# Kernel tuning notes

Hardware: AMD Instinct MI355X
Metric: run time of the kernel (lower is better)

Reference implementation:

```python
import jax, jax.numpy as jnp
import numpy as np

N_SH, N_U, N_I = 1195, 805, 390   # hard-coded in KDHR
D = 64                            # embedding_dim / latent_dim
B = 65536                         # prescription batch
E_SH = 100000
BN_EPS = 1e-5


def setup_inputs() -> dict:
    key = jax.random.key(0)
    ks = jax.random.split(key, 20)
    s = 0.02
    return {
        "edge_index_SH": jax.random.randint(ks[0], (2, E_SH), 0, N_SH),
        "edge_index_SS": jax.random.randint(ks[1], (2, 50000), 0, N_U),
        "edge_index_HH": jax.random.randint(ks[2], (2, 50000), 0, N_I),
        "prescription": jax.random.uniform(ks[3], (B, N_I), dtype=jnp.float32),
        "sh_emb": jax.random.normal(ks[4], (N_SH, D), dtype=jnp.float32) * s,
        # GCNConv_SH layer 1 and 2 (Linear weights, torch layout [out,in])
        "W1": jax.random.normal(ks[5], (D, D), dtype=jnp.float32) * s,
        "b1": jnp.zeros((D,), jnp.float32),
        "W2": jax.random.normal(ks[6], (D, D), dtype=jnp.float32) * s,
        "b2": jnp.zeros((D,), jnp.float32),
        # proj = Linear(64,64) -> ELU -> Linear(64,64)
        "Wp1": jax.random.normal(ks[7], (D, D), dtype=jnp.float32) * s,
        "bp1": jnp.zeros((D,), jnp.float32),
        "Wp2": jax.random.normal(ks[8], (D, D), dtype=jnp.float32) * s,
        "bp2": jnp.zeros((D,), jnp.float32),
        # self.mlp = Linear(64,64); self.SI_bn = BatchNorm1d(64)
        "Wm": jax.random.normal(ks[9], (D, D), dtype=jnp.float32) * s,
        "bm": jnp.zeros((D,), jnp.float32),
        "bn_gamma": jnp.ones((D,), jnp.float32),
        "bn_beta": jnp.zeros((D,), jnp.float32),
    }


def _gcn_layer(x, W, b, src, dst):
    # GCNConv_SH: message = lin(x_j), aggr='mean' at dst, then tanh
    m = x[src] @ W.T + b                                   # [E, D]
    s = jax.ops.segment_sum(m, dst, num_segments=N_SH)     # [N_SH, D]
    cnt = jax.ops.segment_sum(jnp.ones(dst.shape, x.dtype), dst, num_segments=N_SH)
    return jnp.tanh(s / jnp.maximum(cnt, 1.0)[:, None])


def _l2n(z):
    return z / jnp.linalg.norm(z, axis=1, keepdims=True)


def reference(edge_index_SH, edge_index_SS, edge_index_HH, prescription,
              sh_emb, W1, b1, W2, b2, Wp1, bp1, Wp2, bp2, Wm, bm,
              bn_gamma, bn_beta):
    src, dst = edge_index_SH[0], edge_index_SH[1]
    h1 = _gcn_layer(sh_emb, W1, b1, src, dst)
    h2 = _gcn_layer(h1, W2, b2, src, dst)                  # x_SH6
    c_emb_u, c_emb_i = h2[:N_U], h2[N_U:]                  # [805,64], [390,64]

    def proj(z):
        return jax.nn.elu(z @ Wp1.T + bp1) @ Wp2.T + bp2

    # Same2Loss projected+normalized embeddings (c_u: herbs 390, c_i: users 805)
    es = _l2n(proj(c_emb_i))                               # [390, 64]
    eh = _l2n(proj(c_emb_u))                               # [805, 64]

    e_synd = prescription @ es                             # [B, 64]
    pre_sum = jnp.sum(prescription, axis=1, keepdims=True)
    e = e_synd / pre_sum
    e = e @ Wm.T + bm                                      # mlp
    mu = jnp.mean(e, axis=0)                               # BatchNorm1d (train)
    var = jnp.var(e, axis=0)
    e = (e - mu) * jax.lax.rsqrt(var + BN_EPS) * bn_gamma + bn_beta
    e = jax.nn.relu(e)
    return e @ eh.T                                        # [B, 805]
```

## Files before the change

### kernel.cpp

```cpp
#include <hip/hip_runtime.h>
#include <math.h>

#define NSH 1195
#define NU  805
#define NI  390
#define DD  64
#define BROWS 65536
#define ESH 100000
#define KPAD 416
#define NUPAD 832

typedef _Float16 f16;
typedef _Float16 f16x8 __attribute__((ext_vector_type(8)));
typedef float f32x4 __attribute__((ext_vector_type(4)));

#define OFF_AGG   0u
#define OFF_CNT   76480u
#define OFF_H1    77760u
#define OFF_H2    154240u
#define OFF_EH    230720u
#define OFF_ES    282240u
#define OFF_ESWT  307200u
#define OFF_STATS 332160u
#define OFF_BN    332288u
#define OFF_EPRE  332416u

__global__ __launch_bounds__(256) void agg_kernel(const int* __restrict__ edges,
                                                  const float* __restrict__ x,
                                                  float* __restrict__ agg,
                                                  float* __restrict__ cnt,
                                                  int do_cnt) {
    int gid = blockIdx.x * 256 + threadIdx.x;
    int e = gid >> 6;
    int d = gid & 63;
    if (e < ESH) {
        int s = edges[e];
        int t = edges[ESH + e];
        atomicAdd(&agg[t * DD + d], x[s * DD + d]);
        if (do_cnt && d == 0) atomicAdd(&cnt[t], 1.0f);
    }
}

__global__ __launch_bounds__(256) void gcn_transform(const float* __restrict__ agg,
                                                     const float* __restrict__ cnt,
                                                     const float* __restrict__ W,
                                                     const float* __restrict__ b,
                                                     float* __restrict__ out) {
    __shared__ float s_wt[DD * DD];
    __shared__ float s_z[4 * DD];
    int tid = threadIdx.x;
    for (int i = tid; i < DD * DD; i += 256) {
        int j = i >> 6, k = i & 63;
        s_wt[k * DD + j] = W[i];
    }
    int w = tid >> 6, j = tid & 63;
    int node = blockIdx.x * 4 + w;
    bool active = node < NSH;
    s_z[w * DD + j] = active ? agg[node * DD + j] : 0.f;
    __syncthreads();
    float c = active ? cnt[node] : 0.f;
    float acc = c * b[j];
    #pragma unroll 8
    for (int k = 0; k < DD; k++)
        acc = fmaf(s_z[w * DD + k], s_wt[k * DD + j], acc);
    float h = tanhf(acc / fmaxf(c, 1.0f));
    if (active) out[node * DD + j] = h;
}

__global__ __launch_bounds__(256) void proj_kernel(const float* __restrict__ h2,
                                                   const float* __restrict__ Wp1,
                                                   const float* __restrict__ bp1,
                                                   const float* __restrict__ Wp2,
                                                   const float* __restrict__ bp2,
                                                   f16* __restrict__ eh16,
                                                   float* __restrict__ es) {
    __shared__ float s_w1[DD * DD], s_w2[DD * DD];
    __shared__ float s_z[4 * DD], s_t[4 * DD];
    int tid = threadIdx.x;
    for (int i = tid; i < DD * DD; i += 256) {
        int j = i >> 6, k = i & 63;
        s_w1[k * DD + j] = Wp1[i];
        s_w2[k * DD + j] = Wp2[i];
    }
    int w = tid >> 6, j = tid & 63;
    int node = blockIdx.x * 4 + w;
    bool active = node < NSH;
    s_z[w * DD + j] = active ? h2[node * DD + j] : 0.f;
    __syncthreads();
    float acc = bp1[j];
    #pragma unroll 8
    for (int k = 0; k < DD; k++)
        acc = fmaf(s_z[w * DD + k], s_w1[k * DD + j], acc);
    float t = acc > 0.f ? acc : expm1f(acc);
    s_t[w * DD + j] = t;
    __syncthreads();
    float o = bp2[j];
    #pragma unroll 8
    for (int k = 0; k < DD; k++)
        o = fmaf(s_t[w * DD + k], s_w2[k * DD + j], o);
    float sq = o * o;
    #pragma unroll
    for (int off = 1; off < 64; off <<= 1) sq += __shfl_xor(sq, off);
    float r = o / sqrtf(sq);
    if (active) {
        if (node < NU) eh16[node * DD + j] = (f16)r;
        else           es[(node - NU) * DD + j] = r;
    }
}

__global__ __launch_bounds__(256) void projm_kernel(const float* __restrict__ es,
                                                    const float* __restrict__ Wm,
                                                    f16* __restrict__ esWT) {
    __shared__ float s_wt[DD * DD];
    __shared__ float s_z[4 * DD];
    int tid = threadIdx.x;
    for (int i = tid; i < DD * DD; i += 256) {
        int j = i >> 6, k = i & 63;
        s_wt[k * DD + j] = Wm[i];
    }
    int w = tid >> 6, j = tid & 63;
    int r = blockIdx.x * 4 + w;
    bool active = r < NI;
    s_z[w * DD + j] = active ? es[r * DD + j] : 0.f;
    __syncthreads();
    float o = 0.f;
    #pragma unroll 8
    for (int k = 0; k < DD; k++)
        o = fmaf(s_z[w * DD + k], s_wt[k * DD + j], o);
    if (active) esWT[j * KPAD + r] = (f16)o;
}

__global__ __launch_bounds__(256) void synd_mfma(const float* __restrict__ P,
                                                 const f16* __restrict__ esWT,
                                                 const float* __restrict__ bm,
                                                 float* __restrict__ e_pre,
                                                 float* __restrict__ stats) {
    __shared__ float s_stats[128];
    int tid = threadIdx.x;
    if (tid < 128) s_stats[tid] = 0.f;
    __syncthreads();
    int lane = tid & 63, wv = tid >> 6;
    int l15 = lane & 15, lk = lane >> 4;
    int rowbase = blockIdx.x * 128 + wv * 32;

    f32x4 acc[2][4];
    #pragma unroll
    for (int mi = 0; mi < 2; mi++)
        #pragma unroll
        for (int ni = 0; ni < 4; ni++)
            acc[mi][ni] = (f32x4){0.f, 0.f, 0.f, 0.f};
    float rs[2] = {0.f, 0.f};

    const float* pr[2];
    pr[0] = P + (size_t)(rowbase + l15) * NI;
    pr[1] = P + (size_t)(rowbase + 16 + l15) * NI;
    const f16* bp[4];
    #pragma unroll
    for (int ni = 0; ni < 4; ni++)
        bp[ni] = esWT + (size_t)(ni * 16 + l15) * KPAD;

    for (int step = 0; step < 12; step++) {
        int kb = step * 32 + lk * 8;
        f16x8 afr[2];
        #pragma unroll
        for (int mi = 0; mi < 2; mi++) {
            const float* p = pr[mi] + kb;
            float2 q0 = *(const float2*)(p);
            float2 q1 = *(const float2*)(p + 2);
            float2 q2 = *(const float2*)(p + 4);
            float2 q3 = *(const float2*)(p + 6);
            rs[mi] += ((q0.x + q0.y) + (q1.x + q1.y)) + ((q2.x + q2.y) + (q3.x + q3.y));
            f16x8 a;
            a[0] = (f16)q0.x; a[1] = (f16)q0.y; a[2] = (f16)q1.x; a[3] = (f16)q1.y;
            a[4] = (f16)q2.x; a[5] = (f16)q2.y; a[6] = (f16)q3.x; a[7] = (f16)q3.y;
            afr[mi] = a;
        }
        f16x8 bfr[4];
        #pragma unroll
        for (int ni = 0; ni < 4; ni++)
            bfr[ni] = *(const f16x8*)(bp[ni] + kb);
        #pragma unroll
        for (int mi = 0; mi < 2; mi++)
            #pragma unroll
            for (int ni = 0; ni < 4; ni++)
                acc[mi][ni] = __builtin_amdgcn_mfma_f32_16x16x32_f16(
                    afr[mi], bfr[ni], acc[mi][ni], 0, 0, 0);
    }
    {
        f16x8 afr[2];
        #pragma unroll
        for (int mi = 0; mi < 2; mi++) {
            f16x8 a = (f16x8)(f16)0.f;
            if (lk == 0) {
                const float* p = pr[mi] + 384;
                float2 q0 = *(const float2*)(p);
                float2 q1 = *(const float2*)(p + 2);
                float2 q2 = *(const float2*)(p + 4);
                rs[mi] += ((q0.x + q0.y) + (q1.x + q1.y)) + (q2.x + q2.y);
                a[0] = (f16)q0.x; a[1] = (f16)q0.y; a[2] = (f16)q1.x;
                a[3] = (f16)q1.y; a[4] = (f16)q2.x; a[5] = (f16)q2.y;
            }
            afr[mi] = a;
        }
        f16x8 bfr[4];
        #pragma unroll
        for (int ni = 0; ni < 4; ni++)
            bfr[ni] = *(const f16x8*)(bp[ni] + 384 + lk * 8);
        #pragma unroll
        for (int mi = 0; mi < 2; mi++)
            #pragma unroll
            for (int ni = 0; ni < 4; ni++)
                acc[mi][ni] = __builtin_amdgcn_mfma_f32_16x16x32_f16(
                    afr[mi], bfr[ni], acc[mi][ni], 0, 0, 0);
    }

    #pragma unroll
    for (int mi = 0; mi < 2; mi++) {
        rs[mi] += __shfl_xor(rs[mi], 16);
        rs[mi] += __shfl_xor(rs[mi], 32);
    }
    float rsr[2][4];
    #pragma unroll
    for (int mi = 0; mi < 2; mi++)
        #pragma unroll
        for (int j = 0; j < 4; j++)
            rsr[mi][j] = __shfl(rs[mi], lk * 4 + j);

    float bmv[4];
    #pragma unroll
    for (int ni = 0; ni < 4; ni++) bmv[ni] = bm[ni * 16 + l15];

    #pragma unroll
    for (int ni = 0; ni < 4; ni++) {
        float s = 0.f, q = 0.f;
        #pragma unroll
        for (int mi = 0; mi < 2; mi++) {
            #pragma unroll
            for (int j = 0; j < 4; j++) {
                float v = acc[mi][ni][j] / rsr[mi][j] + bmv[ni];
                int row = rowbase + mi * 16 + lk * 4 + j;
                e_pre[(size_t)row * DD + ni * 16 + l15] = v;
                s += v;
                q = fmaf(v, v, q);
            }
        }
        s += __shfl_xor(s, 16); s += __shfl_xor(s, 32);
        q += __shfl_xor(q, 16); q += __shfl_xor(q, 32);
        if (lk == 0) {
            atomicAdd(&s_stats[ni * 16 + l15], s);
            atomicAdd(&s_stats[64 + ni * 16 + l15], q);
        }
    }
    __syncthreads();
    if (tid < 128) atomicAdd(&stats[tid], s_stats[tid]);
}

#define CG0 448
__global__ __launch_bounds__(256) void out_fused(const float* __restrict__ e_pre,
                                                 const f16* __restrict__ eh16,
                                                 const float* __restrict__ stats,
                                                 const float* __restrict__ gamma,
                                                 const float* __restrict__ beta,
                                                 float* __restrict__ out) {
    __shared__ __align__(16) f16 s_eh[CG0 * DD];
    __shared__ float s_bn[128];
    int tid = threadIdx.x;
    int cg = blockIdx.x;
    int nrows = cg == 0 ? CG0 : (NUPAD - CG0);
    int cbase = cg * CG0;

    if (tid < 64) {
        float mu  = stats[tid] * (1.0f / 65536.0f);
        float ex2 = stats[64 + tid] * (1.0f / 65536.0f);
        float var = ex2 - mu * mu;
        float rstd = 1.0f / sqrtf(var + 1e-5f);
        float sc = rstd * gamma[tid];
        s_bn[tid] = sc;
        s_bn[64 + tid] = beta[tid] - mu * sc;
    }

    const uint4* src = (const uint4*)(eh16 + (size_t)cbase * DD);
    int nchunks = nrows * 8;
    for (int c = tid; c < nchunks; c += 256) {
        int row = c >> 3, slot = c & 7;
        uint4 v = src[c];
        *(uint4*)&s_eh[row * DD + ((slot ^ (row & 7)) << 3)] = v;
    }
    __syncthreads();

    int lane = tid & 63, w = tid >> 6;
    int l15 = lane & 15, lk = lane >> 4;
    int r0 = blockIdx.y * 64 + w * 16;

    f16x8 afr[2];
    {
        const float* pr = e_pre + (size_t)(r0 + l15) * DD;
        #pragma unroll
        for (int ks = 0; ks < 2; ks++) {
            int kb = ks * 32 + lk * 8;
            f32x4 v0 = *(const f32x4*)&pr[kb];
            f32x4 v1 = *(const f32x4*)&pr[kb + 4];
            f16x8 a;
            #pragma unroll
            for (int i = 0; i < 4; i++) {
                a[i]     = (f16)fmaxf(fmaf(v0[i], s_bn[kb + i],     s_bn[64 + kb + i]),     0.f);
                a[4 + i] = (f16)fmaxf(fmaf(v1[i], s_bn[kb + 4 + i], s_bn[64 + kb + 4 + i]), 0.f);
            }
            afr[ks] = a;
        }
    }

    int nt = cg == 0 ? 7 : 6;
    for (int cb = 0; cb < nt; cb += 4) {
        f32x4 acc[4][4];
        #pragma unroll
        for (int tt = 0; tt < 4; tt++)
            #pragma unroll
            for (int c16 = 0; c16 < 4; c16++)
                acc[tt][c16] = (f32x4){0.f, 0.f, 0.f, 0.f};

        #pragma unroll
        for (int tt = 0; tt < 4; tt++) {
            if (cb + tt < nt) {
                #pragma unroll
                for (int c16 = 0; c16 < 4; c16++) {
                    int lc = (cb + tt) * 64 + c16 * 16 + l15;
                    #pragma unroll
                    for (int ks = 0; ks < 2; ks++) {
                        int slot = (ks * 4 + lk) ^ (lc & 7);
                        f16x8 b = *(const f16x8*)&s_eh[lc * DD + (slot << 3)];
                        acc[tt][c16] = __builtin_amdgcn_mfma_f32_16x16x32_f16(
                            afr[ks], b, acc[tt][c16], 0, 0, 0);
                    }
                }
            }
        }
        #pragma unroll
        for (int tt = 0; tt < 4; tt++) {
            if (cb + tt < nt) {
                #pragma unroll
                for (int c16 = 0; c16 < 4; c16++) {
                    int col = cbase + (cb + tt) * 64 + c16 * 16 + l15;
                    if (col < NU) {
                        #pragma unroll
                        for (int j = 0; j < 4; j++) {
                            int row = r0 + lk * 4 + j;
                            out[(size_t)row * NU + col] = acc[tt][c16][j];
                        }
                    }
                }
            }
        }
    }
}

extern "C" void kernel_launch(void* const* d_in, const int* in_sizes, int n_in,
                              void* d_out, int out_size, void* d_ws, size_t ws_size,
                              hipStream_t stream) {
    const int*   eSH   = (const int*)d_in[0];
    const float* presc = (const float*)d_in[3];
    const float* shemb = (const float*)d_in[4];
    const float* W1  = (const float*)d_in[5];
    const float* b1  = (const float*)d_in[6];
    const float* W2  = (const float*)d_in[7];
    const float* b2  = (const float*)d_in[8];
    const float* Wp1 = (const float*)d_in[9];
    const float* bp1 = (const float*)d_in[10];
    const float* Wp2 = (const float*)d_in[11];
    const float* bp2 = (const float*)d_in[12];
    const float* Wm  = (const float*)d_in[13];
    const float* bm  = (const float*)d_in[14];
    const float* gam = (const float*)d_in[15];
    const float* bet = (const float*)d_in[16];

    float* ws    = (float*)d_ws;
    float* agg   = ws + OFF_AGG;
    float* cnt   = ws + OFF_CNT;
    float* h1    = ws + OFF_H1;
    float* h2    = ws + OFF_H2;
    f16*   eh16  = (f16*)(ws + OFF_EH);
    float* es    = ws + OFF_ES;
    f16*   esWT  = (f16*)(ws + OFF_ESWT);
    float* stats = ws + OFF_STATS;
    float* e_pre = ws + OFF_EPRE;
    float* out   = (float*)d_out;

    hipMemsetAsync(agg, 0, (76480 + 1280) * sizeof(float), stream);
    hipMemsetAsync(stats, 0, 128 * sizeof(float), stream);
    hipMemsetAsync(eh16, 0, (size_t)NUPAD * DD * sizeof(f16), stream);
    hipMemsetAsync(esWT, 0, (size_t)DD * KPAD * sizeof(f16), stream);

    agg_kernel<<<25000, 256, 0, stream>>>(eSH, shemb, agg, cnt, 1);
    gcn_transform<<<299, 256, 0, stream>>>(agg, cnt, W1, b1, h1);
    hipMemsetAsync(agg, 0, 76480 * sizeof(float), stream);
    agg_kernel<<<25000, 256, 0, stream>>>(eSH, h1, agg, cnt, 0);
    gcn_transform<<<299, 256, 0, stream>>>(agg, cnt, W2, b2, h2);
    proj_kernel<<<299, 256, 0, stream>>>(h2, Wp1, bp1, Wp2, bp2, eh16, es);
    projm_kernel<<<98, 256, 0, stream>>>(es, Wm, esWT);
    synd_mfma<<<512, 256, 0, stream>>>(presc, esWT, bm, e_pre, stats);
    out_fused<<<dim3(2, 1024), 256, 0, stream>>>(e_pre, eh16, stats, gam, bet, out);
}
```

Measured before the change: 231.7 us.

## Replace atomic edge scatter with CSR gather and fuse GCN layer 2 with projections

Builds a CSR (histogram, scan, scatter) of the SH edges once, so each node gathers its neighbours' features instead of doing 6.4M float atomics per layer. The second GCN layer, the projection MLP, the normalisation and the Wm projection are fused into one per-node kernel, and the memsets are merged into one. The cost is three small serial setup kernels, including a single-block scan, plus one block per node with possibly uneven degrees. Summation order inside each node now follows the order edges land in the CSR, not the atomic order.

```diff
diff --git a/kernel.cpp b/kernel.cpp
--- a/kernel.cpp
+++ b/kernel.cpp
@@ -14,120 +14,163 @@
 typedef _Float16 f16x8 __attribute__((ext_vector_type(8)));
 typedef float f32x4 __attribute__((ext_vector_type(4)));
 
-#define OFF_AGG   0u
-#define OFF_CNT   76480u
-#define OFF_H1    77760u
-#define OFF_H2    154240u
-#define OFF_EH    230720u
-#define OFF_ES    282240u
-#define OFF_ESWT  307200u
-#define OFF_STATS 332160u
-#define OFF_BN    332288u
-#define OFF_EPRE  332416u
-
-__global__ __launch_bounds__(256) void agg_kernel(const int* __restrict__ edges,
-                                                  const float* __restrict__ x,
-                                                  float* __restrict__ agg,
-                                                  float* __restrict__ cnt,
-                                                  int do_cnt) {
-    int gid = blockIdx.x * 256 + threadIdx.x;
-    int e = gid >> 6;
-    int d = gid & 63;
+#define OFF_STATS  0u
+#define OFF_ESWT   128u
+#define OFF_EH     13440u
+#define OFF_HIST   40064u
+#define ZERO_FLOATS 41344u
+#define OFF_ROWPTR 41344u
+#define OFF_CURSOR 42624u
+#define OFF_COLIDX 43904u
+#define OFF_H1     144000u
+#define OFF_EPRE   220480u
+
+__global__ __launch_bounds__(256) void hist_kernel(const int* __restrict__ edges,
+                                                   int* __restrict__ hist) {
+    int e = blockIdx.x * 256 + threadIdx.x;
+    if (e < ESH) atomicAdd(&hist[edges[ESH + e]], 1);
+}
+
+__global__ __launch_bounds__(1024) void scan_kernel(const int* __restrict__ hist,
+                                                    int* __restrict__ row_ptr,
+                                                    int* __restrict__ cursor) {
+    __shared__ int s[2048];
+    int t = threadIdx.x;
+    s[t] = (t < NSH) ? hist[t] : 0;
+    s[t + 1024] = (t + 1024 < NSH) ? hist[t + 1024] : 0;
+    __syncthreads();
+    for (int off = 1; off < 2048; off <<= 1) {
+        int a = s[t], b = s[t + 1024];
+        int aa = (t >= off) ? s[t - off] : 0;
+        int bb = s[t + 1024 - off];
+        __syncthreads();
+        s[t] = a + aa;
+        s[t + 1024] = b + bb;
+        __syncthreads();
+    }
+    if (t == 0) row_ptr[0] = 0;
+    for (int i = t; i < NSH; i += 1024) {
+        row_ptr[i + 1] = s[i];
+        cursor[i] = (i == 0) ? 0 : s[i - 1];
+    }
+}
+
+__global__ __launch_bounds__(256) void scatter_kernel(const int* __restrict__ edges,
+                                                      int* __restrict__ cursor,
+                                                      int* __restrict__ col_idx) {
+    int e = blockIdx.x * 256 + threadIdx.x;
     if (e < ESH) {
-        int s = edges[e];
         int t = edges[ESH + e];
-        atomicAdd(&agg[t * DD + d], x[s * DD + d]);
-        if (do_cnt && d == 0) atomicAdd(&cnt[t], 1.0f);
-    }
-}
-
-__global__ __launch_bounds__(256) void gcn_transform(const float* __restrict__ agg,
-                                                     const float* __restrict__ cnt,
-                                                     const float* __restrict__ W,
-                                                     const float* __restrict__ b,
-                                                     float* __restrict__ out) {
+        int pos = atomicAdd(&cursor[t], 1);
+        col_idx[pos] = edges[e];
+    }
+}
+
+__global__ __launch_bounds__(256) void gcn_gather1(const int* __restrict__ row_ptr,
+                                                   const int* __restrict__ col_idx,
+                                                   const float* __restrict__ x,
+                                                   const float* __restrict__ W,
+                                                   const float* __restrict__ b,
+                                                   float* __restrict__ out) {
     __shared__ float s_wt[DD * DD];
-    __shared__ float s_z[4 * DD];
+    __shared__ float s_p[4 * DD];
     int tid = threadIdx.x;
+    int w = tid >> 6, lane = tid & 63;
     for (int i = tid; i < DD * DD; i += 256) {
         int j = i >> 6, k = i & 63;
         s_wt[k * DD + j] = W[i];
     }
-    int w = tid >> 6, j = tid & 63;
-    int node = blockIdx.x * 4 + w;
-    bool active = node < NSH;
-    s_z[w * DD + j] = active ? agg[node * DD + j] : 0.f;
-    __syncthreads();
-    float c = active ? cnt[node] : 0.f;
-    float acc = c * b[j];
+    int node = blockIdx.x;
+    int beg = row_ptr[node], end = row_ptr[node + 1];
+    float acc = 0.f;
+    for (int e = beg + w; e < end; e += 4)
+        acc += x[col_idx[e] * DD + lane];
+    s_p[w * DD + lane] = acc;
+    __syncthreads();
+    float z = s_p[lane] + s_p[DD + lane] + s_p[2 * DD + lane] + s_p[3 * DD + lane];
+    __syncthreads();
+    if (w == 0) s_p[lane] = z;
+    __syncthreads();
+    float cntf = (float)(end - beg);
+    float o = cntf * b[lane];
     #pragma unroll 8
     for (int k = 0; k < DD; k++)
-        acc = fmaf(s_z[w * DD + k], s_wt[k * DD + j], acc);
-    float h = tanhf(acc / fmaxf(c, 1.0f));
-    if (active) out[node * DD + j] = h;
-}
-
-__global__ __launch_bounds__(256) void proj_kernel(const float* __restrict__ h2,
-                                                   const float* __restrict__ Wp1,
-                                                   const float* __restrict__ bp1,
-                                                   const float* __restrict__ Wp2,
-                                                   const float* __restrict__ bp2,
-                                                   f16* __restrict__ eh16,
-                                                   float* __restrict__ es) {
-    __shared__ float s_w1[DD * DD], s_w2[DD * DD];
-    __shared__ float s_z[4 * DD], s_t[4 * DD];
+        o = fmaf(s_p[k], s_wt[k * DD + lane], o);
+    float h = tanhf(o / fmaxf(cntf, 1.f));
+    if (w == 0) out[node * DD + lane] = h;
+}
+
+__global__ __launch_bounds__(256) void gcn2_fused(const int* __restrict__ row_ptr,
+                                                  const int* __restrict__ col_idx,
+                                                  const float* __restrict__ h1,
+                                                  const float* __restrict__ W2,
+                                                  const float* __restrict__ b2,
+                                                  const float* __restrict__ Wp1,
+                                                  const float* __restrict__ bp1,
+                                                  const float* __restrict__ Wp2,
+                                                  const float* __restrict__ bp2,
+                                                  const float* __restrict__ Wm,
+                                                  f16* __restrict__ eh16,
+                                                  f16* __restrict__ esWT) {
+    __shared__ float s_w2[DD * DD], s_p1[DD * DD], s_p2[DD * DD], s_wm[DD * DD];
+    __shared__ float s_v[4 * DD];
     int tid = threadIdx.x;
+    int w = tid >> 6, lane = tid & 63;
     for (int i = tid; i < DD * DD; i += 256) {
         int j = i >> 6, k = i & 63;
-        s_w1[k * DD + j] = Wp1[i];
-        s_w2[k * DD + j] = Wp2[i];
-    }
-    int w = tid >> 6, j = tid & 63;
-    int node = blockIdx.x * 4 + w;
-    bool active = node < NSH;
-    s_z[w * DD + j] = active ? h2[node * DD + j] : 0.f;
-    __syncthreads();
-    float acc = bp1[j];
+        s_w2[k * DD + j] = W2[i];
+        s_p1[k * DD + j] = Wp1[i];
+        s_p2[k * DD + j] = Wp2[i];
+        s_wm[k * DD + j] = Wm[i];
+    }
+    int node = blockIdx.x;
+    int beg = row_ptr[node], end = row_ptr[node + 1];
+    float acc = 0.f;
+    for (int e = beg + w; e < end; e += 4)
+        acc += h1[col_idx[e] * DD + lane];
+    s_v[w * DD + lane] = acc;
+    __syncthreads();
+    float z = s_v[lane] + s_v[DD + lane] + s_v[2 * DD + lane] + s_v[3 * DD + lane];
+    __syncthreads();
+    if (w == 0) s_v[lane] = z;
+    __syncthreads();
+    float cntf = (float)(end - beg);
+    float o = cntf * b2[lane];
     #pragma unroll 8
     for (int k = 0; k < DD; k++)
-        acc = fmaf(s_z[w * DD + k], s_w1[k * DD + j], acc);
-    float t = acc > 0.f ? acc : expm1f(acc);
-    s_t[w * DD + j] = t;
-    __syncthreads();
-    float o = bp2[j];
+        o = fmaf(s_v[k], s_w2[k * DD + lane], o);
+    float h2v = tanhf(o / fmaxf(cntf, 1.f));
+    __syncthreads();
+    if (w == 0) s_v[lane] = h2v;
+    __syncthreads();
+    float t = bp1[lane];
     #pragma unroll 8
     for (int k = 0; k < DD; k++)
-        o = fmaf(s_t[w * DD + k], s_w2[k * DD + j], o);
-    float sq = o * o;
-    #pragma unroll
-    for (int off = 1; off < 64; off <<= 1) sq += __shfl_xor(sq, off);
-    float r = o / sqrtf(sq);
-    if (active) {
-        if (node < NU) eh16[node * DD + j] = (f16)r;
-        else           es[(node - NU) * DD + j] = r;
-    }
-}
-
-__global__ __launch_bounds__(256) void projm_kernel(const float* __restrict__ es,
-                                                    const float* __restrict__ Wm,
-                                                    f16* __restrict__ esWT) {
-    __shared__ float s_wt[DD * DD];
-    __shared__ float s_z[4 * DD];
-    int tid = threadIdx.x;
-    for (int i = tid; i < DD * DD; i += 256) {
-        int j = i >> 6, k = i & 63;
-        s_wt[k * DD + j] = Wm[i];
-    }
-    int w = tid >> 6, j = tid & 63;
-    int r = blockIdx.x * 4 + w;
-    bool active = r < NI;
-    s_z[w * DD + j] = active ? es[r * DD + j] : 0.f;
-    __syncthreads();
-    float o = 0.f;
+        t = fmaf(s_v[k], s_p1[k * DD + lane], t);
+    t = t > 0.f ? t : expm1f(t);
+    __syncthreads();
+    if (w == 0) s_v[lane] = t;
+    __syncthreads();
+    float o2 = bp2[lane];
     #pragma unroll 8
     for (int k = 0; k < DD; k++)
-        o = fmaf(s_z[w * DD + k], s_wt[k * DD + j], o);
-    if (active) esWT[j * KPAD + r] = (f16)o;
+        o2 = fmaf(s_v[k], s_p2[k * DD + lane], o2);
+    float sq = o2 * o2;
+    #pragma unroll
+    for (int off = 1; off < 64; off <<= 1) sq += __shfl_xor(sq, off);
+    float r = o2 / sqrtf(sq);
+    if (node < NU) {
+        if (w == 0) eh16[node * DD + lane] = (f16)r;
+    } else {
+        __syncthreads();
+        if (w == 0) s_v[lane] = r;
+        __syncthreads();
+        float m = 0.f;
+        #pragma unroll 8
+        for (int k = 0; k < DD; k++)
+            m = fmaf(s_v[k], s_wm[k * DD + lane], m);
+        if (w == 0) esWT[lane * KPAD + (node - NU)] = (f16)m;
+    }
 }
 
 __global__ __launch_bounds__(256) void synd_mfma(const float* __restrict__ P,
@@ -374,29 +417,25 @@
     const float* bet = (const float*)d_in[16];
 
     float* ws    = (float*)d_ws;
-    float* agg   = ws + OFF_AGG;
-    float* cnt   = ws + OFF_CNT;
+    float* stats = ws + OFF_STATS;
+    f16*   esWT  = (f16*)(ws + OFF_ESWT);
+    f16*   eh16  = (f16*)(ws + OFF_EH);
+    int*   hist  = (int*)(ws + OFF_HIST);
+    int*   rowp  = (int*)(ws + OFF_ROWPTR);
+    int*   curs  = (int*)(ws + OFF_CURSOR);
+    int*   cidx  = (int*)(ws + OFF_COLIDX);
     float* h1    = ws + OFF_H1;
-    float* h2    = ws + OFF_H2;
-    f16*   eh16  = (f16*)(ws + OFF_EH);
-    float* es    = ws + OFF_ES;
-    f16*   esWT  = (f16*)(ws + OFF_ESWT);
-    float* stats = ws + OFF_STATS;
     float* e_pre = ws + OFF_EPRE;
     float* out   = (float*)d_out;
 
-    hipMemsetAsync(agg, 0, (76480 + 1280) * sizeof(float), stream);
-    hipMemsetAsync(stats, 0, 128 * sizeof(float), stream);
-    hipMemsetAsync(eh16, 0, (size_t)NUPAD * DD * sizeof(f16), stream);
-    hipMemsetAsync(esWT, 0, (size_t)DD * KPAD * sizeof(f16), stream);
-
-    agg_kernel<<<25000, 256, 0, stream>>>(eSH, shemb, agg, cnt, 1);
-    gcn_transform<<<299, 256, 0, stream>>>(agg, cnt, W1, b1, h1);
-    hipMemsetAsync(agg, 0, 76480 * sizeof(float), stream);
-    agg_kernel<<<25000, 256, 0, stream>>>(eSH, h1, agg, cnt, 0);
-    gcn_transform<<<299, 256, 0, stream>>>(agg, cnt, W2, b2, h2);
-    proj_kernel<<<299, 256, 0, stream>>>(h2, Wp1, bp1, Wp2, bp2, eh16, es);
-    projm_kernel<<<98, 256, 0, stream>>>(es, Wm, esWT);
+    hipMemsetAsync(ws, 0, ZERO_FLOATS * sizeof(float), stream);
+
+    hist_kernel<<<391, 256, 0, stream>>>(eSH, hist);
+    scan_kernel<<<1, 1024, 0, stream>>>(hist, rowp, curs);
+    scatter_kernel<<<391, 256, 0, stream>>>(eSH, curs, cidx);
+    gcn_gather1<<<NSH, 256, 0, stream>>>(rowp, cidx, shemb, W1, b1, h1);
+    gcn2_fused<<<NSH, 256, 0, stream>>>(rowp, cidx, h1, W2, b2,
+                                        Wp1, bp1, Wp2, bp2, Wm, eh16, esWT);
     synd_mfma<<<512, 256, 0, stream>>>(presc, esWT, bm, e_pre, stats);
     out_fused<<<dim3(2, 1024), 256, 0, stream>>>(e_pre, eh16, stats, gam, bet, out);
 }
```

Measured after the change: 231.0 us. Within noise of the previous version (-0.3%).
